# Kernel tuning notes

Measured on AMD Instinct MI355X. Metric: run time of the kernel, lower is better.

## Reference

```python
import jax, jax.numpy as jnp
import numpy as np
from jax import lax

B, V, H, W = 8, 3, 512, 640


def setup_inputs() -> dict:
    key = jax.random.key(0)
    k1, k2, k3 = jax.random.split(key, 3)
    # predicted depths in a realistic positive range
    pred_pts = jax.random.uniform(k1, (B, V, H, W), jnp.float32, 1.0, 10.0)
    # pinhole intrinsics embedded in 4x4 (invertible)
    f = 500.0
    K1 = jnp.array([[f, 0.0, (W - 1) / 2.0, 0.0],
                    [0.0, f, (H - 1) / 2.0, 0.0],
                    [0.0, 0.0, 1.0, 0.0],
                    [0.0, 0.0, 0.0, 1.0]], jnp.float32)
    K = jnp.broadcast_to(K1, (B, 4, 4))
    # near-identity rotations (QR of I + small noise) + small translations
    A = jnp.eye(3, dtype=jnp.float32) + 0.05 * jax.random.normal(k2, (B, V, 3, 3), jnp.float32)
    Q, R = jnp.linalg.qr(A)
    Q = Q * jnp.sign(jnp.diagonal(R, axis1=-2, axis2=-1))[..., None, :]
    t = 0.1 * jax.random.normal(k3, (B, V, 3), jnp.float32)
    RT = (jnp.zeros((B, V, 4, 4), jnp.float32)
          .at[..., :3, :3].set(Q)
          .at[..., :3, 3].set(t)
          .at[..., 3, 3].set(1.0))
    return {"pred_pts": pred_pts, "K": K, "input_RTs": RT}


def _bilinear_sample(img_flat, gx, gy, h, w):
    """grid_sample(mode=bilinear, align_corners=False, padding=zeros).
    img_flat: (B, H*W); gx, gy: (B, N) in [-1, 1] grid coords."""
    ix = ((gx + 1.0) * w - 1.0) * 0.5
    iy = ((gy + 1.0) * h - 1.0) * 0.5
    x0f = jnp.floor(ix)
    y0f = jnp.floor(iy)
    wx1 = ix - x0f
    wy1 = iy - y0f
    x0 = x0f.astype(jnp.int32)
    y0 = y0f.astype(jnp.int32)

    def corner(xi, yi):
        valid = (xi >= 0) & (xi < w) & (yi >= 0) & (yi < h)
        idx = jnp.clip(yi, 0, h - 1) * w + jnp.clip(xi, 0, w - 1)
        val = jnp.take_along_axis(img_flat, idx, axis=1)
        return jnp.where(valid, val, 0.0)

    return ((1.0 - wy1) * (1.0 - wx1) * corner(x0, y0)
            + (1.0 - wy1) * wx1 * corner(x0 + 1, y0)
            + wy1 * (1.0 - wx1) * corner(x0, y0 + 1)
            + wy1 * wx1 * corner(x0 + 1, y0 + 1))


def reference(pred_pts, K, input_RTs):
    b, v, h, w = pred_pts.shape
    dt = pred_pts.dtype
    yy, xx = jnp.meshgrid(jnp.arange(h, dtype=dt), jnp.arange(w, dtype=dt), indexing='ij')
    x = xx.reshape(-1)  # (HW,)
    y = yy.reshape(-1)
    Kinv = jnp.linalg.inv(K)            # (B,4,4)
    RTinv = jnp.linalg.inv(input_RTs)   # (B,V,4,4)

    total = jnp.zeros((), dt)
    for i in range(v):
        for j in range(v):
            d = pred_pts[:, i].reshape(b, -1)          # (B, HW)
            ones = jnp.ones_like(d)
            # homogeneous coords (x*d, y*d, d, 1): (B, 4, HW)
            xyz = jnp.stack([x[None] * d, y[None] * d, d, ones], axis=1)
            # composed projection: K @ RT_j @ inv(RT_i) @ inv(K)  (same math as chained bmms)
            P = jnp.einsum('bij,bjk,bkl,blm->bim', K, input_RTs[:, j], RTinv[:, i], Kinv)
            proj = jnp.einsum('bij,bjn->bin', P, xyz)  # (B, 4, HW)
            proj = proj / proj[:, 3:4]
            projected_depth = proj[:, 2]               # (B, HW)
            gx = proj[:, 0] / ((w - 1) / 2.0) - 1.0
            gy = proj[:, 1] / ((h - 1) / 2.0) - 1.0
            mask = ((gx >= -1.0) & (gx <= 1.0) & (gy >= -1.0) & (gy <= 1.0)).astype(dt)
            warped = _bilinear_sample(pred_pts[:, j].reshape(b, -1), gx, gy, h, w)
            num = jnp.sum(jnp.abs(warped - projected_depth) * mask)
            den = jnp.maximum(jnp.sum(mask), 1.0)
            total = total + num / den
    return total
```

## Files before the change

kernel.cpp:

```cpp
#include <hip/hip_runtime.h>

#define Bn 8
#define Vn 3
#define Hn 512
#define Wn 640
#define Nn (Hn * Wn)
#define PX 16
#define TPB 256
#define XBLKS (Nn / (TPB * PX))
#define GRIDN (XBLKS * Vn * Bn)

struct __attribute__((aligned(4))) fpair { float a, b; };

__device__ __forceinline__ float rfl(float x) {
    return __int_as_float(__builtin_amdgcn_readfirstlane(__float_as_int(x)));
}

__device__ __forceinline__ void computeQ(const float* __restrict__ K,
                                         const float* __restrict__ RT,
                                         int b, int i, float Q[Vn][12]) {
    const float* Kb = K + (size_t)b * 16;
    const float f  = Kb[0], cx = Kb[2], cy = Kb[6];
    const float rf = 1.0f / f;
    const float* Ti = RT + (size_t)(b * Vn + i) * 16;
    const float A00=Ti[0], A01=Ti[1], A02=Ti[2],  A03=Ti[3];
    const float A10=Ti[4], A11=Ti[5], A12=Ti[6],  A13=Ti[7];
    const float A20=Ti[8], A21=Ti[9], A22=Ti[10], A23=Ti[11];
    const float I00=A00, I01=A10, I02=A20, I03=-(A00*A03 + A10*A13 + A20*A23);
    const float I10=A01, I11=A11, I12=A21, I13=-(A01*A03 + A11*A13 + A21*A23);
    const float I20=A02, I21=A12, I22=A22, I23=-(A02*A03 + A12*A13 + A22*A23);
    #pragma unroll
    for (int j = 0; j < Vn; ++j) {
        const float* Tj = RT + (size_t)(b * Vn + j) * 16;
        const float B00=Tj[0], B01=Tj[1], B02=Tj[2],  B03=Tj[3];
        const float B10=Tj[4], B11=Tj[5], B12=Tj[6],  B13=Tj[7];
        const float B20=Tj[8], B21=Tj[9], B22=Tj[10], B23=Tj[11];
        const float M00=B00*I00+B01*I10+B02*I20, M01=B00*I01+B01*I11+B02*I21,
                    M02=B00*I02+B01*I12+B02*I22, M03=B00*I03+B01*I13+B02*I23+B03;
        const float M10=B10*I00+B11*I10+B12*I20, M11=B10*I01+B11*I11+B12*I21,
                    M12=B10*I02+B11*I12+B12*I22, M13=B10*I03+B11*I13+B12*I23+B13;
        const float M20=B20*I00+B21*I10+B22*I20, M21=B20*I01+B21*I11+B22*I21,
                    M22=B20*I02+B21*I12+B22*I22, M23=B20*I03+B21*I13+B22*I23+B23;
        const float G00=f*M00+cx*M20, G01=f*M01+cx*M21, G02=f*M02+cx*M22, G03=f*M03+cx*M23;
        const float G10=f*M10+cy*M20, G11=f*M11+cy*M21, G12=f*M12+cy*M22, G13=f*M13+cy*M23;
        const float G20=M20,          G21=M21,          G22=M22,          G23=M23;
        Q[j][0]  = rfl(G00*rf);  Q[j][1]  = rfl(G01*rf);
        Q[j][2]  = rfl(G02 - (cx*rf)*G00 - (cy*rf)*G01);  Q[j][3]  = rfl(G03);
        Q[j][4]  = rfl(G10*rf);  Q[j][5]  = rfl(G11*rf);
        Q[j][6]  = rfl(G12 - (cx*rf)*G10 - (cy*rf)*G11);  Q[j][7]  = rfl(G13);
        Q[j][8]  = rfl(G20*rf);  Q[j][9]  = rfl(G21*rf);
        Q[j][10] = rfl(G22 - (cx*rf)*G20 - (cy*rf)*G21);  Q[j][11] = rfl(G23);
    }
}

__global__ __launch_bounds__(TPB, 8) void loss_main_kernel(const float* __restrict__ pred,
                                                           const float* __restrict__ K,
                                                           const float* __restrict__ RT,
                                                           float* __restrict__ part) {
    const int id   = blockIdx.x;
    const int b    = id & 7;
    const int r    = id >> 3;
    const int i    = r % Vn;
    const int xblk = r / Vn;

    float Q[Vn][12];
    computeQ(K, RT, b, i, Q);

    const int p    = threadIdx.x * XBLKS + xblk;
    const int base = p * PX;
    const int yrow = base / Wn;
    const int xcol = base - yrow * Wn;
    const float fy = (float)yrow;

    const float* dptr = pred + (size_t)(b * Vn + i) * Nn + base;
    float dv[PX];
    {
        const float4 a0 = *reinterpret_cast<const float4*>(dptr);
        const float4 a1 = *reinterpret_cast<const float4*>(dptr + 4);
        const float4 a2 = *reinterpret_cast<const float4*>(dptr + 8);
        const float4 a3 = *reinterpret_cast<const float4*>(dptr + 12);
        dv[0]=a0.x; dv[1]=a0.y; dv[2]=a0.z; dv[3]=a0.w;
        dv[4]=a1.x; dv[5]=a1.y; dv[6]=a1.z; dv[7]=a1.w;
        dv[8]=a2.x; dv[9]=a2.y; dv[10]=a2.z; dv[11]=a2.w;
        dv[12]=a3.x; dv[13]=a3.y; dv[14]=a3.z; dv[15]=a3.w;
    }

    const float cW = (float)Wn / (float)(Wn - 1);
    const float cH = (float)Hn / (float)(Hn - 1);

    float num[Vn] = {0.0f, 0.0f, 0.0f};
    float den[Vn] = {0.0f, 0.0f, 0.0f};

    #pragma unroll
    for (int j = 0; j < Vn; ++j) {
        const float* __restrict__ img = pred + (size_t)(b * Vn + j) * Nn;
        const float rx = fmaf(Q[j][1], fy, Q[j][2]);
        const float ry = fmaf(Q[j][5], fy, Q[j][6]);
        const float rz = fmaf(Q[j][9], fy, Q[j][10]);

        #pragma unroll
        for (int k = 0; k < PX; ++k) {
            const float d  = dv[k];
            const float fx = (float)(xcol + k);

            const float X = fmaf(d, fmaf(Q[j][0], fx, rx), Q[j][3]);
            const float Y = fmaf(d, fmaf(Q[j][4], fx, ry), Q[j][7]);
            const float Z = fmaf(d, fmaf(Q[j][8], fx, rz), Q[j][11]);

            const bool inb = (X >= 0.0f) & (X <= (float)(Wn - 1)) &
                             (Y >= 0.0f) & (Y <= (float)(Hn - 1));
            if (inb) {
                const float ix = fmaf(X, cW, -0.5f);
                const float iy = fmaf(Y, cH, -0.5f);
                const float x0f = floorf(ix);
                const float y0f = floorf(iy);
                const float wx1 = ix - x0f;
                const float wy1 = iy - y0f;
                const float wx0 = 1.0f - wx1;
                const float wy0 = 1.0f - wy1;
                const int x0 = (int)x0f;
                const int y0 = (int)y0f;
                const bool border = (x0 < 0) | (x0 > Wn - 2) | (y0 < 0) | (y0 > Hn - 2);
                float warped;
                if (__ballot(border) == 0ull) {
                    const int ad = y0 * Wn + x0;
                    const fpair q0 = *reinterpret_cast<const fpair*>(img + ad);
                    const fpair q1 = *reinterpret_cast<const fpair*>(img + ad + Wn);
                    warped = wy0 * fmaf(wx0, q0.a, wx1 * q0.b)
                           + wy1 * fmaf(wx0, q1.a, wx1 * q1.b);
                } else {
                    const int x1 = x0 + 1;
                    const int y1 = y0 + 1;
                    const int cy0 = max(y0, 0);
                    const int cy1 = min(y1, Hn - 1);
                    const int cx  = min(max(x0, 0), Wn - 2);
                    const bool xlo = (x0 >= 0);
                    const bool xhi = (x0 <= Wn - 2);
                    const fpair q0 = *reinterpret_cast<const fpair*>(img + (cy0 * Wn + cx));
                    const fpair q1 = *reinterpret_cast<const fpair*>(img + (cy1 * Wn + cx));
                    const float c00 = xhi ? q0.a : q0.b;
                    const float c10 = xlo ? q0.b : q0.a;
                    const float c01 = xhi ? q1.a : q1.b;
                    const float c11 = xlo ? q1.b : q1.a;
                    const float wx0v = xlo ? wx0 : 0.0f;
                    const float wx1v = (x1 < Wn) ? wx1 : 0.0f;
                    const float wy0v = (y0 >= 0) ? wy0 : 0.0f;
                    const float wy1v = (y1 < Hn) ? wy1 : 0.0f;
                    warped = wy0v * fmaf(wx0v, c00, wx1v * c10)
                           + wy1v * fmaf(wx0v, c01, wx1v * c11);
                }
                num[j] += fabsf(warped - Z);
                den[j] += 1.0f;
            }
        }
    }

    #pragma unroll
    for (int off = 32; off > 0; off >>= 1) {
        #pragma unroll
        for (int j = 0; j < Vn; ++j) {
            num[j] += __shfl_down(num[j], off, 64);
            den[j] += __shfl_down(den[j], off, 64);
        }
    }
    __shared__ float s_red[4][2 * Vn];
    const int lane = threadIdx.x & 63;
    const int wid  = threadIdx.x >> 6;
    if (lane == 0) {
        #pragma unroll
        for (int j = 0; j < Vn; ++j) {
            s_red[wid][2 * j + 0] = num[j];
            s_red[wid][2 * j + 1] = den[j];
        }
    }
    __syncthreads();
    if (threadIdx.x < 2 * Vn) {
        const int slot = threadIdx.x;
        const float v = s_red[0][slot] + s_red[1][slot] + s_red[2][slot] + s_red[3][slot];
        part[(size_t)id * 8 + slot] = v;
    }
}

__global__ __launch_bounds__(TPB) void finalize_kernel(const float* __restrict__ part,
                                                       float* __restrict__ out) {
    float acc[2 * Vn * Vn];
    #pragma unroll
    for (int s = 0; s < 2 * Vn * Vn; ++s) acc[s] = 0.0f;

    for (int m = threadIdx.x; m < GRIDN; m += TPB) {
        const int i = (m >> 3) % Vn;
        const float* pp = part + (size_t)m * 8;
        #pragma unroll
        for (int j = 0; j < Vn; ++j) {
            acc[(i * Vn + j) * 2 + 0] += pp[2 * j + 0];
            acc[(i * Vn + j) * 2 + 1] += pp[2 * j + 1];
        }
    }
    #pragma unroll
    for (int off = 32; off > 0; off >>= 1) {
        #pragma unroll
        for (int s = 0; s < 2 * Vn * Vn; ++s)
            acc[s] += __shfl_down(acc[s], off, 64);
    }
    __shared__ float s_fin[4][2 * Vn * Vn];
    const int lane = threadIdx.x & 63;
    const int wid  = threadIdx.x >> 6;
    if (lane == 0) {
        #pragma unroll
        for (int s = 0; s < 2 * Vn * Vn; ++s) s_fin[wid][s] = acc[s];
    }
    __syncthreads();
    if (threadIdx.x == 0) {
        float t = 0.0f;
        #pragma unroll
        for (int pr = 0; pr < Vn * Vn; ++pr) {
            const float nn = s_fin[0][pr*2+0] + s_fin[1][pr*2+0] + s_fin[2][pr*2+0] + s_fin[3][pr*2+0];
            const float dd = s_fin[0][pr*2+1] + s_fin[1][pr*2+1] + s_fin[2][pr*2+1] + s_fin[3][pr*2+1];
            t += nn / fmaxf(dd, 1.0f);
        }
        out[0] = t;
    }
}

extern "C" void kernel_launch(void* const* d_in, const int* in_sizes, int n_in,
                              void* d_out, int out_size, void* d_ws, size_t ws_size,
                              hipStream_t stream) {
    const float* pred = (const float*)d_in[0];
    const float* K    = (const float*)d_in[1];
    const float* RT   = (const float*)d_in[2];
    float* out = (float*)d_out;

    float* part = (float*)d_ws;

    loss_main_kernel<<<GRIDN, TPB, 0, stream>>>(pred, K, RT, part);
    finalize_kernel<<<1, TPB, 0, stream>>>(part, out);
}
```

Baseline: 111.4 us.

## Interleave target views per pixel to batch gathers and split depth loads

Loop order is swapped so that each source pixel projects into all three target views at once, and the six bilinear gathers are issued together before any arithmetic. This should expose more memory-level parallelism per thread and use one ballot per pixel instead of one per view. Depth values are now loaded in two halves of eight, which lowers peak register pressure. Out-of-bounds views are masked arithmetically and read a dummy address 0, which adds redundant loads and wastes work when only some views are valid.

Measured after the change: 132.0 us. +18.6%, slower.

```diff
diff --git a/kernel.cpp b/kernel.cpp
--- a/kernel.cpp
+++ b/kernel.cpp
@@ -72,85 +72,131 @@
     const int xcol = base - yrow * Wn;
     const float fy = (float)yrow;
 
-    const float* dptr = pred + (size_t)(b * Vn + i) * Nn + base;
-    float dv[PX];
-    {
-        const float4 a0 = *reinterpret_cast<const float4*>(dptr);
-        const float4 a1 = *reinterpret_cast<const float4*>(dptr + 4);
-        const float4 a2 = *reinterpret_cast<const float4*>(dptr + 8);
-        const float4 a3 = *reinterpret_cast<const float4*>(dptr + 12);
-        dv[0]=a0.x; dv[1]=a0.y; dv[2]=a0.z; dv[3]=a0.w;
-        dv[4]=a1.x; dv[5]=a1.y; dv[6]=a1.z; dv[7]=a1.w;
-        dv[8]=a2.x; dv[9]=a2.y; dv[10]=a2.z; dv[11]=a2.w;
-        dv[12]=a3.x; dv[13]=a3.y; dv[14]=a3.z; dv[15]=a3.w;
-    }
+    const float* dbase = pred + (size_t)(b * Vn + i) * Nn + base;
 
     const float cW = (float)Wn / (float)(Wn - 1);
     const float cH = (float)Hn / (float)(Hn - 1);
 
+    float rx[Vn], ry[Vn], rz[Vn];
+    #pragma unroll
+    for (int j = 0; j < Vn; ++j) {
+        rx[j] = fmaf(Q[j][1], fy, Q[j][2]);
+        ry[j] = fmaf(Q[j][5], fy, Q[j][6]);
+        rz[j] = fmaf(Q[j][9], fy, Q[j][10]);
+    }
+
     float num[Vn] = {0.0f, 0.0f, 0.0f};
     float den[Vn] = {0.0f, 0.0f, 0.0f};
 
     #pragma unroll
-    for (int j = 0; j < Vn; ++j) {
-        const float* __restrict__ img = pred + (size_t)(b * Vn + j) * Nn;
-        const float rx = fmaf(Q[j][1], fy, Q[j][2]);
-        const float ry = fmaf(Q[j][5], fy, Q[j][6]);
-        const float rz = fmaf(Q[j][9], fy, Q[j][10]);
-
-        #pragma unroll
-        for (int k = 0; k < PX; ++k) {
+    for (int half = 0; half < 2; ++half) {
+        float dv[8];
+        {
+            const float4 a0 = *reinterpret_cast<const float4*>(dbase + half * 8);
+            const float4 a1 = *reinterpret_cast<const float4*>(dbase + half * 8 + 4);
+            dv[0]=a0.x; dv[1]=a0.y; dv[2]=a0.z; dv[3]=a0.w;
+            dv[4]=a1.x; dv[5]=a1.y; dv[6]=a1.z; dv[7]=a1.w;
+        }
+        #pragma unroll
+        for (int k = 0; k < 8; ++k) {
             const float d  = dv[k];
-            const float fx = (float)(xcol + k);
-
-            const float X = fmaf(d, fmaf(Q[j][0], fx, rx), Q[j][3]);
-            const float Y = fmaf(d, fmaf(Q[j][4], fx, ry), Q[j][7]);
-            const float Z = fmaf(d, fmaf(Q[j][8], fx, rz), Q[j][11]);
-
-            const bool inb = (X >= 0.0f) & (X <= (float)(Wn - 1)) &
-                             (Y >= 0.0f) & (Y <= (float)(Hn - 1));
-            if (inb) {
-                const float ix = fmaf(X, cW, -0.5f);
-                const float iy = fmaf(Y, cH, -0.5f);
-                const float x0f = floorf(ix);
-                const float y0f = floorf(iy);
-                const float wx1 = ix - x0f;
-                const float wy1 = iy - y0f;
-                const float wx0 = 1.0f - wx1;
-                const float wy0 = 1.0f - wy1;
-                const int x0 = (int)x0f;
-                const int y0 = (int)y0f;
-                const bool border = (x0 < 0) | (x0 > Wn - 2) | (y0 < 0) | (y0 > Hn - 2);
-                float warped;
-                if (__ballot(border) == 0ull) {
-                    const int ad = y0 * Wn + x0;
-                    const fpair q0 = *reinterpret_cast<const fpair*>(img + ad);
-                    const fpair q1 = *reinterpret_cast<const fpair*>(img + ad + Wn);
-                    warped = wy0 * fmaf(wx0, q0.a, wx1 * q0.b)
-                           + wy1 * fmaf(wx0, q1.a, wx1 * q1.b);
+            const float fx = (float)(xcol + half * 8 + k);
+
+            float Za[Vn];
+            bool  ia[Vn];
+            float ixa[Vn], iya[Vn];
+            #pragma unroll
+            for (int j = 0; j < Vn; ++j) {
+                const float X = fmaf(d, fmaf(Q[j][0], fx, rx[j]), Q[j][3]);
+                const float Y = fmaf(d, fmaf(Q[j][4], fx, ry[j]), Q[j][7]);
+                Za[j] = fmaf(d, fmaf(Q[j][8], fx, rz[j]), Q[j][11]);
+                ia[j] = (X >= 0.0f) & (X <= (float)(Wn - 1)) &
+                        (Y >= 0.0f) & (Y <= (float)(Hn - 1));
+                ixa[j] = fmaf(X, cW, -0.5f);
+                iya[j] = fmaf(Y, cH, -0.5f);
+            }
+
+            if (ia[0] | ia[1] | ia[2]) {
+                float wx1a[Vn], wy1a[Vn];
+                int   x0a[Vn], y0a[Vn];
+                bool  bord = false;
+                #pragma unroll
+                for (int j = 0; j < Vn; ++j) {
+                    const float x0f = floorf(ixa[j]);
+                    const float y0f = floorf(iya[j]);
+                    wx1a[j] = ixa[j] - x0f;
+                    wy1a[j] = iya[j] - y0f;
+                    x0a[j] = (int)x0f;
+                    y0a[j] = (int)y0f;
+                    bord |= ia[j] & ((x0a[j] < 0) | (x0a[j] > Wn - 2) |
+                                     (y0a[j] < 0) | (y0a[j] > Hn - 2));
+                }
+
+                if (__ballot(bord) == 0ull) {
+                    int ad[Vn];
+                    #pragma unroll
+                    for (int j = 0; j < Vn; ++j)
+                        ad[j] = ia[j] ? (y0a[j] * Wn + x0a[j]) : 0;
+                    fpair q0[Vn], q1[Vn];
+                    #pragma unroll
+                    for (int j = 0; j < Vn; ++j) {
+                        const float* img = pred + (size_t)(b * Vn + j) * Nn;
+                        q0[j] = *reinterpret_cast<const fpair*>(img + ad[j]);
+                        q1[j] = *reinterpret_cast<const fpair*>(img + ad[j] + Wn);
+                    }
+                    #pragma unroll
+                    for (int j = 0; j < Vn; ++j) {
+                        const float wx1 = wx1a[j], wy1 = wy1a[j];
+                        const float wx0 = 1.0f - wx1, wy0 = 1.0f - wy1;
+                        const float wx0v = ia[j] ? wx0 : 0.0f;
+                        const float wx1v = ia[j] ? wx1 : 0.0f;
+                        const float warped = wy0 * fmaf(wx0v, q0[j].a, wx1v * q0[j].b)
+                                           + wy1 * fmaf(wx0v, q1[j].a, wx1v * q1[j].b);
+                        const float Zs = ia[j] ? Za[j] : 0.0f;
+                        num[j] += fabsf(warped - Zs);
+                        den[j] += ia[j] ? 1.0f : 0.0f;
+                    }
                 } else {
-                    const int x1 = x0 + 1;
-                    const int y1 = y0 + 1;
-                    const int cy0 = max(y0, 0);
-                    const int cy1 = min(y1, Hn - 1);
-                    const int cx  = min(max(x0, 0), Wn - 2);
-                    const bool xlo = (x0 >= 0);
-                    const bool xhi = (x0 <= Wn - 2);
-                    const fpair q0 = *reinterpret_cast<const fpair*>(img + (cy0 * Wn + cx));
-                    const fpair q1 = *reinterpret_cast<const fpair*>(img + (cy1 * Wn + cx));
-                    const float c00 = xhi ? q0.a : q0.b;
-                    const float c10 = xlo ? q0.b : q0.a;
-                    const float c01 = xhi ? q1.a : q1.b;
-                    const float c11 = xlo ? q1.b : q1.a;
-                    const float wx0v = xlo ? wx0 : 0.0f;
-                    const float wx1v = (x1 < Wn) ? wx1 : 0.0f;
-                    const float wy0v = (y0 >= 0) ? wy0 : 0.0f;
-                    const float wy1v = (y1 < Hn) ? wy1 : 0.0f;
-                    warped = wy0v * fmaf(wx0v, c00, wx1v * c10)
-                           + wy1v * fmaf(wx0v, c01, wx1v * c11);
+                    int  r0[Vn], r1[Vn];
+                    bool xlo[Vn], xhi[Vn];
+                    #pragma unroll
+                    for (int j = 0; j < Vn; ++j) {
+                        const int y1 = y0a[j] + 1;
+                        const int cx2 = min(max(x0a[j], 0), Wn - 2);
+                        const int cy0 = min(max(y0a[j], 0), Hn - 1);
+                        const int cy1 = min(max(y1, 0), Hn - 1);
+                        r0[j] = cy0 * Wn + cx2;
+                        r1[j] = cy1 * Wn + cx2;
+                        xlo[j] = (x0a[j] >= 0);
+                        xhi[j] = (x0a[j] <= Wn - 2);
+                    }
+                    fpair q0[Vn], q1[Vn];
+                    #pragma unroll
+                    for (int j = 0; j < Vn; ++j) {
+                        const float* img = pred + (size_t)(b * Vn + j) * Nn;
+                        q0[j] = *reinterpret_cast<const fpair*>(img + r0[j]);
+                        q1[j] = *reinterpret_cast<const fpair*>(img + r1[j]);
+                    }
+                    #pragma unroll
+                    for (int j = 0; j < Vn; ++j) {
+                        const float wx1 = wx1a[j], wy1 = wy1a[j];
+                        const float wx0 = 1.0f - wx1, wy0 = 1.0f - wy1;
+                        const float c00 = xhi[j] ? q0[j].a : q0[j].b;
+                        const float c10 = xlo[j] ? q0[j].b : q0[j].a;
+                        const float c01 = xhi[j] ? q1[j].a : q1[j].b;
+                        const float c11 = xlo[j] ? q1[j].b : q1[j].a;
+                        const bool inb = ia[j];
+                        const float wx0v = (inb && xlo[j])            ? wx0 : 0.0f;
+                        const float wx1v = (inb && (x0a[j] + 1 < Wn)) ? wx1 : 0.0f;
+                        const float wy0v = (inb && (y0a[j] >= 0))     ? wy0 : 0.0f;
+                        const float wy1v = (inb && (y0a[j] + 1 < Hn)) ? wy1 : 0.0f;
+                        const float warped = wy0v * fmaf(wx0v, c00, wx1v * c10)
+                                           + wy1v * fmaf(wx0v, c01, wx1v * c11);
+                        const float Zs = inb ? Za[j] : 0.0f;
+                        num[j] += fabsf(warped - Zs);
+                        den[j] += inb ? 1.0f : 0.0f;
+                    }
                 }
-                num[j] += fabsf(warped - Z);
-                den[j] += 1.0f;
             }
         }
     }
```
